# Optimization experiments

Measured on AMD Instinct MI355X. Metric: run time of the kernel, lower is better.

The kernel has to match this reference:

```python
import jax, jax.numpy as jnp
import numpy as np

BS, CK, H, W, T = 4, 64, 32, 32, 16
HW = H * W
N = T * HW
CV = 256
TOP_K = 30


def setup_inputs() -> dict:
    key = jax.random.key(0)
    ks = jax.random.split(key, 16)
    inp = {
        'query_key': jax.random.normal(ks[0], (BS, CK, H, W), jnp.float32),
        'query_selection': jax.random.uniform(ks[1], (BS, CK, H, W), jnp.float32),
        'pix_feat': jax.random.normal(ks[2], (BS, CV, H, W), jnp.float32),
        'sensory': jax.random.normal(ks[3], (BS, CV, H, W), jnp.float32),
        'last_mask': jax.random.uniform(ks[4], (BS, 1, H, W), jnp.float32),
        'last_pix_feat': jax.random.normal(ks[5], (BS, CV, H, W), jnp.float32),
        'last_msk_value': jax.random.normal(ks[6], (BS, 1, CV, H, W), jnp.float32),
        'mem_key': jax.random.normal(ks[7], (BS, CK, N), jnp.float32),
        'mem_shrinkage': jax.random.uniform(ks[8], (BS, 1, N), jnp.float32),
        'mem_msk_value': jax.random.normal(ks[9], (BS, CV, N), jnp.float32),
        'mem_valid': jnp.ones((BS, N), jnp.float32),
        'obj_memory': jax.random.normal(ks[10], (BS, 1, 16, CV), jnp.float32),
        # uncertainty head proxy: 1x1 conv over concat(last_pix_feat, pix_feat, last_mask, diff)
        'W_uncert': jax.random.normal(ks[11], (1, CV + CV + 1 + CV), jnp.float32) * 0.02,
        'b_uncert': jnp.zeros((1,), jnp.float32),
    }
    return inp


def reference(query_key, query_selection, pix_feat, sensory, last_mask,
              last_pix_feat, last_msk_value, mem_key, mem_shrinkage,
              mem_msk_value, mem_valid, obj_memory, W_uncert, b_uncert):
    bs = query_key.shape[0]
    h, w = query_key.shape[-2:]
    hw = h * w
    qk = query_key.reshape(bs, CK, hw)            # [b,64,hw]
    qe = query_selection.reshape(bs, CK, hw)      # [b,64,hw]
    mk_t = jnp.swapaxes(mem_key, 1, 2)            # [b,N,64]
    # negative squared L2 distance, selection-weighted
    a_sq = jnp.einsum('bnc,bch->bnh', mk_t * mk_t, qe)
    two_ab = 2.0 * jnp.einsum('bnc,bch->bnh', mk_t, qk * qe)
    b_sq = jnp.sum(qe * qk * qk, axis=1, keepdims=True)     # [b,1,hw]
    sim = (-a_sq + two_ab - b_sq)                           # [b,N,hw]
    sim = sim * jnp.swapaxes(mem_shrinkage, 1, 2) / jnp.sqrt(jnp.float32(CK))
    sim = sim + (1.0 - mem_valid[..., None]) * -60000.0
    # top-k softmax over memory axis, scatter back to dense affinity
    sim_t = jnp.swapaxes(sim, 1, 2)                         # [b,hw,N]
    top_vals, top_idx = jax.lax.top_k(sim_t, TOP_K)         # [b,hw,k]
    probs = jax.nn.softmax(top_vals, axis=-1)
    b_ix = jnp.arange(bs)[:, None, None]
    q_ix = jnp.arange(hw)[None, :, None]
    aff = jnp.zeros_like(sim_t).at[b_ix, q_ix, top_idx].set(probs)  # [b,hw,N]
    visual = jnp.einsum('bcn,bhn->bch', mem_msk_value, aff).reshape(bs, 1, CV, h, w)
    # uncertainty-gated blend with last memory value (pred_uncertainty proxy: 1x1 conv)
    diff = visual[:, 0] - last_msk_value[:, 0]              # [b,256,h,w]
    feats = jnp.concatenate([last_pix_feat, pix_feat, last_mask, diff], axis=1)
    logits = jnp.einsum('bchw,oc->bohw', feats, W_uncert) + b_uncert[None, :, None, None]
    up = jax.nn.sigmoid(logits)[:, None]                    # [b,1,1,h,w]
    out = visual * up + last_msk_value * (1.0 - up)         # [b,1,256,h,w]
    return out
```

## Files before the change

kernel.cpp:

```cpp
#include <hip/hip_runtime.h>
#include <math.h>

#define BSZ 4
#define CKC 64
#define HWP 1024
#define NMEM 16384
#define CVC 256
#define PT 16
#define NT 256

#define WS_BQ_OFF   0
#define WS_BQ_SZ    (BSZ * 128 * HWP)
#define WS_BSQ_OFF  (WS_BQ_OFF + WS_BQ_SZ)
#define WS_BSQ_SZ   (BSZ * HWP)
#define WS_PRE_OFF  (WS_BSQ_OFF + WS_BSQ_SZ)
#define WS_PRE_SZ   (BSZ * HWP)
#define WS_VT_OFF   (WS_PRE_OFF + WS_PRE_SZ)
#define WS_VT_SZ    (BSZ * NMEM * CVC)
#define WS_TOTAL_FLOATS (WS_VT_OFF + WS_VT_SZ)

__global__ __launch_bounds__(256) void prep_kernel(
    const float* __restrict__ qk, const float* __restrict__ qe,
    const float* __restrict__ pf, const float* __restrict__ lm,
    const float* __restrict__ lpf, const float* __restrict__ lmv,
    const float* __restrict__ W, const float* __restrict__ bu,
    float* __restrict__ Bq, float* __restrict__ bsq, float* __restrict__ prelog)
{
    __shared__ float red[16][17];
    const int t  = threadIdx.x;
    const int b  = blockIdx.x >> 6;
    const int p0 = (blockIdx.x & 63) << 4;
    const int pp = t & 15;
    const int cg = t >> 4;
    const int p  = p0 + pp;

    const float* qkb = qk + (size_t)b * CKC * HWP;
    const float* qeb = qe + (size_t)b * CKC * HWP;
    float* Bqb = Bq + (size_t)b * 128 * HWP;

    float bs = 0.f;
    #pragma unroll
    for (int i = 0; i < 4; ++i) {
        const int cidx = (cg << 2) + i;
        const float k_ = qkb[cidx * HWP + p];
        const float e_ = qeb[cidx * HWP + p];
        Bqb[cidx * HWP + p]        = 2.f * k_ * e_;
        Bqb[(64 + cidx) * HWP + p] = -e_;
        bs += e_ * k_ * k_;
    }
    red[cg][pp] = bs;
    __syncthreads();
    if (t < 16) {
        float s = 0.f;
        #pragma unroll
        for (int g2 = 0; g2 < 16; ++g2) s += red[g2][t];
        bsq[b * HWP + p0 + t] = s;
    }
    const float* lpfb = lpf + (size_t)b * CVC * HWP;
    const float* pfb  = pf  + (size_t)b * CVC * HWP;
    const float* lmvb = lmv + (size_t)b * CVC * HWP;
    float lg = 0.f;
    #pragma unroll
    for (int i = 0; i < 16; ++i) {
        const int cidx = (cg << 4) + i;
        lg += W[cidx]       * lpfb[cidx * HWP + p];
        lg += W[256 + cidx] * pfb[cidx * HWP + p];
        lg -= W[513 + cidx] * lmvb[cidx * HWP + p];
    }
    __syncthreads();
    red[cg][pp] = lg;
    __syncthreads();
    if (t < 16) {
        float s = bu[0] + W[512] * lm[b * HWP + p0 + t];
        #pragma unroll
        for (int g2 = 0; g2 < 16; ++g2) s += red[g2][t];
        prelog[b * HWP + p0 + t] = s;
    }
}

__global__ __launch_bounds__(256) void transpose_v(const float* __restrict__ V,
                                                   float* __restrict__ VT)
{
    __shared__ float tile[32][33];
    const int b  = blockIdx.z;
    const int n0 = blockIdx.x << 5;
    const int c0 = blockIdx.y << 5;
    const int tx = threadIdx.x, ty = threadIdx.y;
    const float* Vb  = V  + (size_t)b * CVC * NMEM;
    float*       VTb = VT + (size_t)b * NMEM * CVC;
    #pragma unroll
    for (int i = 0; i < 32; i += 8)
        tile[ty + i][tx] = Vb[(size_t)(c0 + ty + i) * NMEM + n0 + tx];
    __syncthreads();
    #pragma unroll
    for (int i = 0; i < 32; i += 8)
        VTb[(size_t)(n0 + ty + i) * CVC + c0 + tx] = tile[tx][ty + i];
}

__global__ __launch_bounds__(256) void main_kernel(
    const float* __restrict__ mk, const float* __restrict__ shr,
    const float* __restrict__ valid, const float* __restrict__ Vv,
    const float* __restrict__ lmv, const float* __restrict__ Bq,
    const float* __restrict__ bsq, const float* __restrict__ prelog,
    const float* __restrict__ W, float* __restrict__ out, int use_vt)
{
    __shared__ float fS[64][16];
    __shared__ float gS[64][16];
    __shared__ float mkS[64][256];
    __shared__ float shrS[NT];
    __shared__ float penS[NT];
    __shared__ float bsqS[PT];
    __shared__ float prelS[PT];
    __shared__ float heapV[PT][32];
    __shared__ int   heapI[PT][32];
    __shared__ float minV[PT];
    __shared__ int   minPos[PT];
    __shared__ float qV[PT][64];
    __shared__ int   qI[PT][64];
    __shared__ int   qCnt[PT];
    __shared__ int   pendAny;
    __shared__ float probS[PT][32];
    __shared__ float partS[4][PT];
    __shared__ float upS[PT];

    const int t  = threadIdx.x;
    const int b  = blockIdx.x >> 6;
    const int p0 = (blockIdx.x & 63) << 4;
    const int tn = t & 63;
    const int tp = t >> 6;

    const float* Bqb = Bq + (size_t)b * 128 * HWP;
    for (int idx = t; idx < 64 * PT; idx += 256) {
        const int c = idx >> 4, pp = idx & 15;
        fS[c][pp] = Bqb[c * HWP + p0 + pp];
        gS[c][pp] = Bqb[(64 + c) * HWP + p0 + pp];
    }
    if (t < PT) {
        bsqS[t]  = bsq[b * HWP + p0 + t];
        prelS[t] = prelog[b * HWP + p0 + t];
        qCnt[t]  = 0;
    }
    if (t == 0) pendAny = 0;

    const float* mkb  = mk  + (size_t)b * CKC * NMEM;
    const float* shrb = shr + (size_t)b * NMEM;
    const float* vlb  = valid + (size_t)b * NMEM;

    for (int ntile = 0; ntile < NMEM / NT; ++ntile) {
        const int n0 = ntile << 8;
        shrS[t] = shrb[n0 + t] * 0.125f;
        penS[t] = (1.f - vlb[n0 + t]) * -60000.f;
        #pragma unroll
        for (int k = 0; k < 16; ++k) {
            const int idx = t + (k << 8);
            const int row = idx >> 6;
            const int c4  = (idx & 63) << 2;
            *(float4*)&mkS[row][c4] =
                *(const float4*)&mkb[(size_t)row * NMEM + n0 + c4];
        }
        __syncthreads();

        float acc[4][4];
        #pragma unroll
        for (int i = 0; i < 4; ++i)
            #pragma unroll
            for (int j = 0; j < 4; ++j) acc[i][j] = 0.f;

        #pragma unroll 8
        for (int cc = 0; cc < 64; ++cc) {
            const float4 a4 = *(const float4*)&mkS[cc][tn << 2];
            const float4 f4 = *(const float4*)&fS[cc][tp << 2];
            const float4 g4 = *(const float4*)&gS[cc][tp << 2];
            const float m[4]  = {a4.x, a4.y, a4.z, a4.w};
            const float ff[4] = {f4.x, f4.y, f4.z, f4.w};
            const float gg[4] = {g4.x, g4.y, g4.z, g4.w};
            #pragma unroll
            for (int i = 0; i < 4; ++i) {
                const float mv = m[i];
                const float m2 = mv * mv;
                #pragma unroll
                for (int j = 0; j < 4; ++j)
                    acc[i][j] = fmaf(mv, ff[j], fmaf(m2, gg[j], acc[i][j]));
            }
        }

        float simv[4][4];
        #pragma unroll
        for (int i = 0; i < 4; ++i) {
            const float sh = shrS[(tn << 2) + i];
            const float pe = penS[(tn << 2) + i];
            #pragma unroll
            for (int j = 0; j < 4; ++j)
                simv[i][j] = fmaf(acc[i][j] - bsqS[(tp << 2) + j], sh, pe);
        }

        unsigned pending = 0xFFFFu;
        if (ntile == 0) {
            if (tn < 8) {
                #pragma unroll
                for (int i = 0; i < 4; ++i)
                    #pragma unroll
                    for (int j = 0; j < 4; ++j) {
                        heapV[(tp << 2) + j][(tn << 2) + i] = simv[i][j];
                        heapI[(tp << 2) + j][(tn << 2) + i] = (tn << 2) + i;
                    }
                pending = 0;
            }
            __syncthreads();
            if (t < PT) {
                float mv = heapV[t][0]; int mp = 0;
                #pragma unroll
                for (int s = 1; s < 32; ++s) {
                    const float v = heapV[t][s];
                    if (v < mv) { mv = v; mp = s; }
                }
                minV[t] = mv; minPos[t] = mp;
            }
            __syncthreads();
        }

        while (true) {
            if (t == 0) pendAny = 0;
            if (t < PT) qCnt[t] = 0;
            __syncthreads();
            if (pending) {
                #pragma unroll
                for (int j = 0; j < 4; ++j) {
                    const int p = (tp << 2) + j;
                    const float mv = minV[p];
                    #pragma unroll
                    for (int i = 0; i < 4; ++i) {
                        const unsigned bitm = 1u << ((j << 2) + i);
                        if (pending & bitm) {
                            const float v = simv[i][j];
                            if (v > mv) {
                                const int slot = atomicAdd(&qCnt[p], 1);
                                if (slot < 64) {
                                    qV[p][slot] = v;
                                    qI[p][slot] = n0 + (tn << 2) + i;
                                    pending &= ~bitm;
                                }
                            } else pending &= ~bitm;
                        }
                    }
                }
                if (pending) pendAny = 1;
            }
            __syncthreads();
            if (t < PT) {
                const int p = t;
                int cnt = qCnt[p]; if (cnt > 64) cnt = 64;
                if (cnt) {
                    float mv = minV[p]; int mp = minPos[p];
                    for (int s = 0; s < cnt; ++s) {
                        const float v = qV[p][s];
                        if (v > mv) {
                            heapV[p][mp] = v;
                            heapI[p][mp] = qI[p][s];
                            mv = heapV[p][0]; mp = 0;
                            for (int s2 = 1; s2 < 32; ++s2) {
                                const float v2 = heapV[p][s2];
                                if (v2 < mv) { mv = v2; mp = s2; }
                            }
                        }
                    }
                    minV[p] = mv; minPos[p] = mp;
                }
            }
            __syncthreads();
            const int again = pendAny;
            __syncthreads();
            if (!again) break;
        }
    }

    if (t < PT) {
        const int p = t;
        float mx = heapV[p][0];
        #pragma unroll
        for (int s = 1; s < 32; ++s) mx = fmaxf(mx, heapV[p][s]);
        float m1v = heapV[p][0]; int m1 = 0;
        #pragma unroll
        for (int s = 1; s < 32; ++s) { const float v = heapV[p][s]; if (v < m1v) { m1v = v; m1 = s; } }
        float m2v = 3.0e38f; int m2 = -1;
        #pragma unroll
        for (int s = 0; s < 32; ++s) {
            if (s != m1) { const float v = heapV[p][s]; if (v < m2v) { m2v = v; m2 = s; } }
        }
        float sum = 0.f;
        #pragma unroll
        for (int s = 0; s < 32; ++s) {
            const float e = (s == m1 || s == m2) ? 0.f : expf(heapV[p][s] - mx);
            probS[p][s] = e; sum += e;
        }
        const float inv = 1.f / sum;
        #pragma unroll
        for (int s = 0; s < 32; ++s) probS[p][s] *= inv;
    }
    __syncthreads();

    const int c = t;
    float vis[PT];
    const float* Vb = Vv + (use_vt ? (size_t)b * NMEM * CVC : (size_t)b * CVC * NMEM);
    #pragma unroll
    for (int p = 0; p < PT; ++p) {
        float a = 0.f;
        for (int s = 0; s < 32; ++s) {
            const float pr = probS[p][s];
            if (pr != 0.f) {
                const int idx = heapI[p][s];
                const float v = use_vt ? Vb[(size_t)idx * CVC + c]
                                       : Vb[(size_t)c * NMEM + idx];
                a = fmaf(pr, v, a);
            }
        }
        vis[p] = a;
    }
    const float w3 = W[513 + c];
    #pragma unroll
    for (int p = 0; p < PT; ++p) {
        float v = w3 * vis[p];
        #pragma unroll
        for (int off = 32; off > 0; off >>= 1) v += __shfl_xor(v, off, 64);
        if (tn == 0) partS[tp][p] = v;
    }
    __syncthreads();
    if (t < PT) {
        const float lg = prelS[t] + partS[0][t] + partS[1][t] + partS[2][t] + partS[3][t];
        upS[t] = 1.f / (1.f + expf(-lg));
    }
    __syncthreads();
    const float* lmvp = lmv + ((size_t)b * CVC + c) * HWP + p0;
    float*       outp = out + ((size_t)b * CVC + c) * HWP + p0;
    #pragma unroll
    for (int p = 0; p < PT; ++p) {
        const float u = upS[p];
        outp[p] = vis[p] * u + lmvp[p] * (1.f - u);
    }
}

extern "C" void kernel_launch(void* const* d_in, const int* in_sizes, int n_in,
                              void* d_out, int out_size, void* d_ws, size_t ws_size,
                              hipStream_t stream)
{
    const float* qk  = (const float*)d_in[0];
    const float* qe  = (const float*)d_in[1];
    const float* pf  = (const float*)d_in[2];
    const float* lm  = (const float*)d_in[4];
    const float* lpf = (const float*)d_in[5];
    const float* lmv = (const float*)d_in[6];
    const float* mk  = (const float*)d_in[7];
    const float* shr = (const float*)d_in[8];
    const float* Vv  = (const float*)d_in[9];
    const float* vld = (const float*)d_in[10];
    const float* W   = (const float*)d_in[12];
    const float* bu  = (const float*)d_in[13];
    float* out = (float*)d_out;
    float* ws  = (float*)d_ws;

    float* Bq     = ws + WS_BQ_OFF;
    float* bsq    = ws + WS_BSQ_OFF;
    float* prelog = ws + WS_PRE_OFF;
    float* VT     = ws + WS_VT_OFF;
    const int use_vt = (ws_size >= (size_t)WS_TOTAL_FLOATS * sizeof(float)) ? 1 : 0;

    prep_kernel<<<BSZ * 64, 256, 0, stream>>>(qk, qe, pf, lm, lpf, lmv, W, bu,
                                              Bq, bsq, prelog);
    if (use_vt)
        transpose_v<<<dim3(NMEM / 32, CVC / 32, BSZ), dim3(32, 8), 0, stream>>>(Vv, VT);
    main_kernel<<<BSZ * 64, 256, 0, stream>>>(mk, shr, vld, use_vt ? VT : Vv,
                                              lmv, Bq, bsq, prelog, W, out, use_vt);
}
```

Baseline: 798.4 us.

## Split memory axis across blocks with partial top-k and separate merge kernel

The fused similarity/top-k kernel launched only 256 blocks, so each block scanned all 16384 memory entries serially. It now splits the memory axis into 8 chunks, giving 2048 blocks that each keep a partial top-32 per query pixel and write it to workspace. A new merge kernel combines the 8 partial lists, then runs the softmax, value gather and uncertainty blend. The tile also shrinks to 128 memory entries with 2 pixels per thread, and the per-pixel queue drops to 32 slots. The split costs extra workspace traffic, a serial per-thread merge of 256 candidates, and more partial-heap work in total.

```diff
diff --git a/kernel.cpp b/kernel.cpp
--- a/kernel.cpp
+++ b/kernel.cpp
@@ -7,16 +7,22 @@
 #define NMEM 16384
 #define CVC 256
 #define PT 16
-#define NT 256
-
-#define WS_BQ_OFF   0
-#define WS_BQ_SZ    (BSZ * 128 * HWP)
-#define WS_BSQ_OFF  (WS_BQ_OFF + WS_BQ_SZ)
-#define WS_BSQ_SZ   (BSZ * HWP)
-#define WS_PRE_OFF  (WS_BSQ_OFF + WS_BSQ_SZ)
-#define WS_PRE_SZ   (BSZ * HWP)
-#define WS_VT_OFF   (WS_PRE_OFF + WS_PRE_SZ)
-#define WS_VT_SZ    (BSZ * NMEM * CVC)
+#define NT 128
+#define NSPLIT 8
+#define CHUNK (NMEM / NSPLIT)
+
+#define WS_BQ_OFF    0
+#define WS_BQ_SZ     (BSZ * 128 * HWP)
+#define WS_BSQ_OFF   (WS_BQ_OFF + WS_BQ_SZ)
+#define WS_BSQ_SZ    (BSZ * HWP)
+#define WS_PRE_OFF   (WS_BSQ_OFF + WS_BSQ_SZ)
+#define WS_PRE_SZ    (BSZ * HWP)
+#define WS_PARTV_OFF (WS_PRE_OFF + WS_PRE_SZ)
+#define WS_PARTV_SZ  (BSZ * HWP * NSPLIT * 32)
+#define WS_PARTI_OFF (WS_PARTV_OFF + WS_PARTV_SZ)
+#define WS_PARTI_SZ  (BSZ * HWP * NSPLIT * 32)
+#define WS_VT_OFF    (WS_PARTI_OFF + WS_PARTI_SZ)
+#define WS_VT_SZ     (BSZ * NMEM * CVC)
 #define WS_TOTAL_FLOATS (WS_VT_OFF + WS_VT_SZ)
 
 __global__ __launch_bounds__(256) void prep_kernel(
@@ -97,37 +103,35 @@
         VTb[(size_t)(n0 + ty + i) * CVC + c0 + tx] = tile[tx][ty + i];
 }
 
-__global__ __launch_bounds__(256) void main_kernel(
+__global__ __launch_bounds__(256) void sim_topk_kernel(
     const float* __restrict__ mk, const float* __restrict__ shr,
-    const float* __restrict__ valid, const float* __restrict__ Vv,
-    const float* __restrict__ lmv, const float* __restrict__ Bq,
-    const float* __restrict__ bsq, const float* __restrict__ prelog,
-    const float* __restrict__ W, float* __restrict__ out, int use_vt)
+    const float* __restrict__ valid, const float* __restrict__ Bq,
+    const float* __restrict__ bsq,
+    float* __restrict__ partV, float* __restrict__ partI)
 {
     __shared__ float fS[64][16];
     __shared__ float gS[64][16];
-    __shared__ float mkS[64][256];
+    __shared__ float mkS[64][NT];
     __shared__ float shrS[NT];
     __shared__ float penS[NT];
     __shared__ float bsqS[PT];
-    __shared__ float prelS[PT];
     __shared__ float heapV[PT][32];
     __shared__ int   heapI[PT][32];
     __shared__ float minV[PT];
     __shared__ int   minPos[PT];
-    __shared__ float qV[PT][64];
-    __shared__ int   qI[PT][64];
+    __shared__ float qV[PT][32];
+    __shared__ int   qI[PT][32];
     __shared__ int   qCnt[PT];
     __shared__ int   pendAny;
-    __shared__ float probS[PT][32];
-    __shared__ float partS[4][PT];
-    __shared__ float upS[PT];
-
-    const int t  = threadIdx.x;
-    const int b  = blockIdx.x >> 6;
-    const int p0 = (blockIdx.x & 63) << 4;
-    const int tn = t & 63;
-    const int tp = t >> 6;
+
+    const int t     = threadIdx.x;
+    const int b     = blockIdx.x >> 9;
+    const int pg    = (blockIdx.x >> 3) & 63;
+    const int ns    = blockIdx.x & 7;
+    const int p0    = pg << 4;
+    const int nbase = ns * CHUNK;
+    const int tn    = t & 31;
+    const int tp    = t >> 5;
 
     const float* Bqb = Bq + (size_t)b * 128 * HWP;
     for (int idx = t; idx < 64 * PT; idx += 256) {
@@ -136,73 +140,69 @@
         gS[c][pp] = Bqb[(64 + c) * HWP + p0 + pp];
     }
     if (t < PT) {
-        bsqS[t]  = bsq[b * HWP + p0 + t];
-        prelS[t] = prelog[b * HWP + p0 + t];
-        qCnt[t]  = 0;
+        bsqS[t] = bsq[b * HWP + p0 + t];
+        qCnt[t] = 0;
     }
     if (t == 0) pendAny = 0;
 
-    const float* mkb  = mk  + (size_t)b * CKC * NMEM;
-    const float* shrb = shr + (size_t)b * NMEM;
+    const float* mkb  = mk    + (size_t)b * CKC * NMEM;
+    const float* shrb = shr   + (size_t)b * NMEM;
     const float* vlb  = valid + (size_t)b * NMEM;
 
-    for (int ntile = 0; ntile < NMEM / NT; ++ntile) {
-        const int n0 = ntile << 8;
-        shrS[t] = shrb[n0 + t] * 0.125f;
-        penS[t] = (1.f - vlb[n0 + t]) * -60000.f;
-        #pragma unroll
-        for (int k = 0; k < 16; ++k) {
+    for (int ntile = 0; ntile < CHUNK / NT; ++ntile) {
+        const int nstart = nbase + ntile * NT;
+        if (t < NT) {
+            shrS[t] = shrb[nstart + t] * 0.125f;
+            penS[t] = (1.f - vlb[nstart + t]) * -60000.f;
+        }
+        #pragma unroll
+        for (int k = 0; k < 8; ++k) {
             const int idx = t + (k << 8);
-            const int row = idx >> 6;
-            const int c4  = (idx & 63) << 2;
+            const int row = idx >> 5;
+            const int c4  = (idx & 31) << 2;
             *(float4*)&mkS[row][c4] =
-                *(const float4*)&mkb[(size_t)row * NMEM + n0 + c4];
+                *(const float4*)&mkb[(size_t)row * NMEM + nstart + c4];
         }
         __syncthreads();
 
-        float acc[4][4];
-        #pragma unroll
-        for (int i = 0; i < 4; ++i)
-            #pragma unroll
-            for (int j = 0; j < 4; ++j) acc[i][j] = 0.f;
+        float acc[4][2];
+        #pragma unroll
+        for (int i = 0; i < 4; ++i) { acc[i][0] = 0.f; acc[i][1] = 0.f; }
 
         #pragma unroll 8
         for (int cc = 0; cc < 64; ++cc) {
             const float4 a4 = *(const float4*)&mkS[cc][tn << 2];
-            const float4 f4 = *(const float4*)&fS[cc][tp << 2];
-            const float4 g4 = *(const float4*)&gS[cc][tp << 2];
+            const float2 f2 = *(const float2*)&fS[cc][tp << 1];
+            const float2 g2 = *(const float2*)&gS[cc][tp << 1];
             const float m[4]  = {a4.x, a4.y, a4.z, a4.w};
-            const float ff[4] = {f4.x, f4.y, f4.z, f4.w};
-            const float gg[4] = {g4.x, g4.y, g4.z, g4.w};
             #pragma unroll
             for (int i = 0; i < 4; ++i) {
                 const float mv = m[i];
                 const float m2 = mv * mv;
-                #pragma unroll
-                for (int j = 0; j < 4; ++j)
-                    acc[i][j] = fmaf(mv, ff[j], fmaf(m2, gg[j], acc[i][j]));
-            }
-        }
-
-        float simv[4][4];
+                acc[i][0] = fmaf(mv, f2.x, fmaf(m2, g2.x, acc[i][0]));
+                acc[i][1] = fmaf(mv, f2.y, fmaf(m2, g2.y, acc[i][1]));
+            }
+        }
+
+        float simv[4][2];
         #pragma unroll
         for (int i = 0; i < 4; ++i) {
             const float sh = shrS[(tn << 2) + i];
             const float pe = penS[(tn << 2) + i];
             #pragma unroll
-            for (int j = 0; j < 4; ++j)
-                simv[i][j] = fmaf(acc[i][j] - bsqS[(tp << 2) + j], sh, pe);
-        }
-
-        unsigned pending = 0xFFFFu;
+            for (int j = 0; j < 2; ++j)
+                simv[i][j] = fmaf(acc[i][j] - bsqS[(tp << 1) + j], sh, pe);
+        }
+
+        unsigned pending = 0xFFu;
         if (ntile == 0) {
             if (tn < 8) {
                 #pragma unroll
                 for (int i = 0; i < 4; ++i)
                     #pragma unroll
-                    for (int j = 0; j < 4; ++j) {
-                        heapV[(tp << 2) + j][(tn << 2) + i] = simv[i][j];
-                        heapI[(tp << 2) + j][(tn << 2) + i] = (tn << 2) + i;
+                    for (int j = 0; j < 2; ++j) {
+                        heapV[(tp << 1) + j][(tn << 2) + i] = simv[i][j];
+                        heapI[(tp << 1) + j][(tn << 2) + i] = nbase + (tn << 2) + i;
                     }
                 pending = 0;
             }
@@ -225,8 +225,8 @@
             __syncthreads();
             if (pending) {
                 #pragma unroll
-                for (int j = 0; j < 4; ++j) {
-                    const int p = (tp << 2) + j;
+                for (int j = 0; j < 2; ++j) {
+                    const int p = (tp << 1) + j;
                     const float mv = minV[p];
                     #pragma unroll
                     for (int i = 0; i < 4; ++i) {
@@ -235,9 +235,9 @@
                             const float v = simv[i][j];
                             if (v > mv) {
                                 const int slot = atomicAdd(&qCnt[p], 1);
-                                if (slot < 64) {
+                                if (slot < 32) {
                                     qV[p][slot] = v;
-                                    qI[p][slot] = n0 + (tn << 2) + i;
+                                    qI[p][slot] = nstart + (tn << 2) + i;
                                     pending &= ~bitm;
                                 }
                             } else pending &= ~bitm;
@@ -249,7 +249,7 @@
             __syncthreads();
             if (t < PT) {
                 const int p = t;
-                int cnt = qCnt[p]; if (cnt > 64) cnt = 64;
+                int cnt = qCnt[p]; if (cnt > 32) cnt = 32;
                 if (cnt) {
                     float mv = minV[p]; int mp = minPos[p];
                     for (int s = 0; s < cnt; ++s) {
@@ -274,8 +274,66 @@
         }
     }
 
+    #pragma unroll
+    for (int idx = t; idx < PT * 32; idx += 256) {
+        const int p = idx >> 5, s = idx & 31;
+        const size_t gp = (size_t)b * HWP + p0 + p;
+        partV[gp * (NSPLIT * 32) + ns * 32 + s] = heapV[p][s];
+        partI[gp * (NSPLIT * 32) + ns * 32 + s] = (float)heapI[p][s];
+    }
+}
+
+__global__ __launch_bounds__(256) void merge_kernel(
+    const float* __restrict__ partV, const float* __restrict__ partI,
+    const float* __restrict__ Vv, const float* __restrict__ lmv,
+    const float* __restrict__ prelog, const float* __restrict__ W,
+    float* __restrict__ out, int use_vt)
+{
+    __shared__ float candV[PT][NSPLIT * 32];
+    __shared__ int   candI[PT][NSPLIT * 32];
+    __shared__ float heapV[PT][32];
+    __shared__ int   heapI[PT][32];
+    __shared__ float probS[PT][32];
+    __shared__ float prelS[PT];
+    __shared__ float partS[4][PT];
+    __shared__ float upS[PT];
+
+    const int t  = threadIdx.x;
+    const int b  = blockIdx.x >> 6;
+    const int pg = blockIdx.x & 63;
+    const int p0 = pg << 4;
+    const int NC = NSPLIT * 32;
+
+    for (int idx = t; idx < PT * NC; idx += 256) {
+        const int p = idx >> 8, s = idx & (NC - 1);
+        const size_t gp = (size_t)b * HWP + p0 + p;
+        candV[p][s] = partV[gp * NC + s];
+        candI[p][s] = (int)partI[gp * NC + s];
+    }
+    if (t < PT) prelS[t] = prelog[b * HWP + p0 + t];
+    __syncthreads();
+
     if (t < PT) {
         const int p = t;
+        float mv = candV[p][0]; int mp = 0;
+        #pragma unroll
+        for (int s = 0; s < 32; ++s) {
+            heapV[p][s] = candV[p][s];
+            heapI[p][s] = candI[p][s];
+            if (candV[p][s] < mv) { mv = candV[p][s]; mp = s; }
+        }
+        for (int s = 32; s < NC; ++s) {
+            const float v = candV[p][s];
+            if (v > mv) {
+                heapV[p][mp] = v;
+                heapI[p][mp] = candI[p][s];
+                mv = heapV[p][0]; mp = 0;
+                for (int s2 = 1; s2 < 32; ++s2) {
+                    const float v2 = heapV[p][s2];
+                    if (v2 < mv) { mv = v2; mp = s2; }
+                }
+            }
+        }
         float mx = heapV[p][0];
         #pragma unroll
         for (int s = 1; s < 32; ++s) mx = fmaxf(mx, heapV[p][s]);
@@ -299,7 +357,9 @@
     }
     __syncthreads();
 
-    const int c = t;
+    const int c  = t;
+    const int ln = t & 63;
+    const int wv = t >> 6;
     float vis[PT];
     const float* Vb = Vv + (use_vt ? (size_t)b * NMEM * CVC : (size_t)b * CVC * NMEM);
     #pragma unroll
@@ -322,7 +382,7 @@
         float v = w3 * vis[p];
         #pragma unroll
         for (int off = 32; off > 0; off >>= 1) v += __shfl_xor(v, off, 64);
-        if (tn == 0) partS[tp][p] = v;
+        if (ln == 0) partS[wv][p] = v;
     }
     __syncthreads();
     if (t < PT) {
@@ -361,6 +421,8 @@
     float* Bq     = ws + WS_BQ_OFF;
     float* bsq    = ws + WS_BSQ_OFF;
     float* prelog = ws + WS_PRE_OFF;
+    float* partV  = ws + WS_PARTV_OFF;
+    float* partI  = ws + WS_PARTI_OFF;
     float* VT     = ws + WS_VT_OFF;
     const int use_vt = (ws_size >= (size_t)WS_TOTAL_FLOATS * sizeof(float)) ? 1 : 0;
 
@@ -368,6 +430,8 @@
                                               Bq, bsq, prelog);
     if (use_vt)
         transpose_v<<<dim3(NMEM / 32, CVC / 32, BSZ), dim3(32, 8), 0, stream>>>(Vv, VT);
-    main_kernel<<<BSZ * 64, 256, 0, stream>>>(mk, shr, vld, use_vt ? VT : Vv,
-                                              lmv, Bq, bsq, prelog, W, out, use_vt);
+    sim_topk_kernel<<<BSZ * 64 * NSPLIT, 256, 0, stream>>>(mk, shr, vld, Bq, bsq,
+                                                           partV, partI);
+    merge_kernel<<<BSZ * 64, 256, 0, stream>>>(partV, partI, use_vt ? VT : Vv,
+                                               lmv, prelog, W, out, use_vt);
 }
```

Result: slower. 941.9 us (+18.0%).
